# Optimization experiments

Hardware: AMD Instinct MI355X
Metric: run time of the kernel (lower is better)

The kernel has to match this reference:

```python
import jax, jax.numpy as jnp
from jax import lax
import numpy as np

B = 1024
CH = 32          # decomp.channel
LEVEL = 3        # decomp.level
CTOT = CH * (LEVEL + 1)   # 128, ODE state dim == GRU input dim
T_POINTS = 96    # decomp.eval_time_points
PRED_LEN = 96
HID = 128


def _dopri5_traj(y0, ts, Wo, bo):
    """Fixed-grid Dormand-Prince 5(4) integration of dy/dt = tanh(y Wo^T + bo).
    y0: [B, CTOT]; ts: [T]. Returns trajectory [T, B, CTOT]."""
    f = lambda y: jnp.tanh(y @ Wo.T + bo)

    def step(y, dt):
        k1 = f(y)
        k2 = f(y + dt * (0.2 * k1))
        k3 = f(y + dt * (3.0 / 40 * k1 + 9.0 / 40 * k2))
        k4 = f(y + dt * (44.0 / 45 * k1 - 56.0 / 15 * k2 + 32.0 / 9 * k3))
        k5 = f(y + dt * (19372.0 / 6561 * k1 - 25360.0 / 2187 * k2 + 64448.0 / 6561 * k3 - 212.0 / 729 * k4))
        k6 = f(y + dt * (9017.0 / 3168 * k1 - 355.0 / 33 * k2 + 46732.0 / 5247 * k3 + 49.0 / 176 * k4 - 5103.0 / 18656 * k5))
        y_next = y + dt * (35.0 / 384 * k1 + 500.0 / 1113 * k3 + 125.0 / 192 * k4 - 2187.0 / 6784 * k5 + 11.0 / 84 * k6)
        return y_next, y_next

    _, ys = lax.scan(step, y0, ts[1:] - ts[:-1])
    return jnp.concatenate([y0[None], ys], axis=0)


def _gru_layer(xs, W_ih, W_hh, b_ih, b_hh):
    """PyTorch-semantics GRU layer. xs: [T, B, D] -> hidden states [T, B, H]."""
    gi = jnp.einsum('tbd,gd->tbg', xs, W_ih) + b_ih  # precompute input gates
    H = W_hh.shape[1]

    def cell(h, gi_t):
        gh = h @ W_hh.T + b_hh
        i_r, i_z, i_n = jnp.split(gi_t, 3, axis=-1)
        h_r, h_z, h_n = jnp.split(gh, 3, axis=-1)
        r = jax.nn.sigmoid(i_r + h_r)
        z = jax.nn.sigmoid(i_z + h_z)
        n = jnp.tanh(i_n + r * h_n)
        h_new = (1.0 - z) * n + z * h
        return h_new, h_new

    h0 = jnp.zeros((xs.shape[1], H), xs.dtype)
    _, hs = lax.scan(cell, h0, gi)
    return hs


def setup_inputs() -> dict:
    key = jax.random.key(0)
    ks = jax.random.split(key, 20)
    s = 0.08  # ~1/sqrt(128), keeps GRU/ODE in a stable regime
    return {
        'x': jax.random.normal(ks[0], (B, CH, 256), jnp.float32),
        'yl': jax.random.normal(ks[1], (B, CH, 1), jnp.float32),
        'yh': jax.random.normal(ks[2], (B, CH * LEVEL, 1), jnp.float32),
        'W_ode': jax.random.normal(ks[3], (CTOT, CTOT), jnp.float32) * 0.05,
        'b_ode': jax.random.normal(ks[4], (CTOT,), jnp.float32) * 0.05,
        'W_ih0': jax.random.normal(ks[5], (3 * HID, CTOT), jnp.float32) * s,
        'W_hh0': jax.random.normal(ks[6], (3 * HID, HID), jnp.float32) * s,
        'b_ih0': jax.random.normal(ks[7], (3 * HID,), jnp.float32) * s,
        'b_hh0': jax.random.normal(ks[8], (3 * HID,), jnp.float32) * s,
        'W_ih1': jax.random.normal(ks[9], (3 * HID, HID), jnp.float32) * s,
        'W_hh1': jax.random.normal(ks[10], (3 * HID, HID), jnp.float32) * s,
        'b_ih1': jax.random.normal(ks[11], (3 * HID,), jnp.float32) * s,
        'b_hh1': jax.random.normal(ks[12], (3 * HID,), jnp.float32) * s,
        'W1': jax.random.normal(ks[13], (64, HID), jnp.float32) * s,
        'b1': jax.random.normal(ks[14], (64,), jnp.float32) * s,
        'W2': jax.random.normal(ks[15], (PRED_LEN * CH, 64), jnp.float32) * 0.125,
        'b2': jax.random.normal(ks[16], (PRED_LEN * CH,), jnp.float32) * 0.125,
    }


def reference(x, yl, yh, W_ode, b_ode,
              W_ih0, W_hh0, b_ih0, b_hh0,
              W_ih1, W_hh1, b_ih1, b_hh1,
              W1, b1, W2, b2):
    # coeffs = cat([yl] + yh, dim=1) -> [B, CTOT, 1] -> squeeze coeff length (=1)
    coeffs = jnp.concatenate([yl, yh], axis=1)[..., 0]  # [B, CTOT]
    ts = jnp.linspace(0.0, 1.0, T_POINTS)
    traj = _dopri5_traj(coeffs, ts, W_ode, b_ode)  # [T, B, CTOT]
    # rearrange 't b c l -> b t (c l)' with l == 1; GRU scans over leading T axis
    h1 = _gru_layer(traj, W_ih0, W_hh0, b_ih0, b_hh0)   # [T, B, HID]
    h2 = _gru_layer(h1, W_ih1, W_hh1, b_ih1, b_hh1)     # [T, B, HID]
    last = h2[-1]                                        # [B, HID]
    hidden = jax.nn.gelu(last @ W1.T + b1, approximate=False)
    pred = hidden @ W2.T + b2                            # [B, PRED_LEN*CH]
    return pred.reshape(-1, CH, PRED_LEN)
```

## Files before the change

### kernel.cpp

```cpp
#include <hip/hip_runtime.h>
#include <hip/hip_bf16.h>
#include <math.h>

#define TPTS 96
#define CTOT 128
#define LDP 134

typedef __bf16 bf16x8_t __attribute__((ext_vector_type(8)));
typedef float f32x4_t __attribute__((ext_vector_type(4)));
typedef unsigned short us8_t __attribute__((ext_vector_type(8)));

__device__ __forceinline__ unsigned short f2b(float f) {
    union { float f; unsigned int i; } v; v.f = f;
    unsigned int r = v.i + 0x7fffu + ((v.i >> 16) & 1u);
    return (unsigned short)(r >> 16);
}
__device__ __forceinline__ unsigned int packbf2(float a, float b) {
    unsigned int r;
    asm("v_cvt_pk_bf16_f32 %0, %1, %2" : "=v"(r) : "v"(a), "v"(b));
    return r;
}
__device__ __forceinline__ uint2 pack4(float v0, float v1, float v2, float v3) {
    uint2 w; w.x = packbf2(v0, v1); w.y = packbf2(v2, v3); return w;
}
__device__ __forceinline__ f32x4_t mfma16(bf16x8_t a, bf16x8_t b, f32x4_t c) {
    return __builtin_amdgcn_mfma_f32_16x16x32_bf16(a, b, c, 0, 0, 0);
}
__device__ __forceinline__ bf16x8_t ldfrag(const unsigned short* p) {
    us8_t v = *(const us8_t*)p;
    return __builtin_bit_cast(bf16x8_t, v);
}
__device__ __forceinline__ bf16x8_t ldfragG(const unsigned short* p) {
    union { unsigned long long q[2]; us8_t v; } u;
    u.q[0] = __hip_atomic_load((const unsigned long long*)p,
                               __ATOMIC_RELAXED, __HIP_MEMORY_SCOPE_AGENT);
    u.q[1] = __hip_atomic_load((const unsigned long long*)(p + 4),
                               __ATOMIC_RELAXED, __HIP_MEMORY_SCOPE_AGENT);
    return __builtin_bit_cast(bf16x8_t, u.v);
}
__device__ __forceinline__ void stg8(unsigned short* p, uint2 pk) {
    unsigned long long q = ((unsigned long long)pk.y << 32) | (unsigned long long)pk.x;
    __hip_atomic_store((unsigned long long*)p, q,
                       __ATOMIC_RELAXED, __HIP_MEMORY_SCOPE_AGENT);
}
__device__ __forceinline__ bf16x8_t ldfragW(const float* p) {
    float4 a = *(const float4*)p;
    float4 b = *(const float4*)(p + 4);
    bf16x8_t r;
    r[0] = __builtin_bit_cast(__bf16, f2b(a.x)); r[1] = __builtin_bit_cast(__bf16, f2b(a.y));
    r[2] = __builtin_bit_cast(__bf16, f2b(a.z)); r[3] = __builtin_bit_cast(__bf16, f2b(a.w));
    r[4] = __builtin_bit_cast(__bf16, f2b(b.x)); r[5] = __builtin_bit_cast(__bf16, f2b(b.y));
    r[6] = __builtin_bit_cast(__bf16, f2b(b.z)); r[7] = __builtin_bit_cast(__bf16, f2b(b.w));
    return r;
}
__device__ __forceinline__ float tanh2(float x) {
    float e = __expf(x + x);
    return 1.f - __fdividef(2.f, e + 1.f);
}
__device__ __forceinline__ float sigm(float x) {
    return __fdividef(1.f, 1.f + __expf(-x));
}

#define LGKM_BAR() do {                                         \
        asm volatile("s_waitcnt lgkmcnt(0)" ::: "memory");      \
        __builtin_amdgcn_s_barrier();                           \
    } while (0)

__device__ __forceinline__ void waitflag(unsigned int* f, unsigned int want) {
    if (threadIdx.x == 0) {
        int guard = 0;
        while (__hip_atomic_load(f, __ATOMIC_RELAXED, __HIP_MEMORY_SCOPE_AGENT) != want) {
            __builtin_amdgcn_s_sleep(1);
            if (++guard > (1 << 22)) break;
        }
    }
    __syncthreads();
}
__device__ __forceinline__ void setflag(unsigned int* f, unsigned int val) {
    if (threadIdx.x == 0) {
        asm volatile("s_waitcnt vmcnt(0)" ::: "memory");
        __hip_atomic_store(f, val, __ATOMIC_RELAXED, __HIP_MEMORY_SCOPE_AGENT);
    }
}

__global__ void __launch_bounds__(512, 2)
ode_forecaster(const float* __restrict__ yl,
               const float* __restrict__ yh,
               const float* __restrict__ Wode,
               const float* __restrict__ bode,
               const float* __restrict__ Wih0,
               const float* __restrict__ Whh0,
               const float* __restrict__ bih0,
               const float* __restrict__ bhh0,
               const float* __restrict__ Wih1,
               const float* __restrict__ Whh1,
               const float* __restrict__ bih1,
               const float* __restrict__ bhh1,
               const float* __restrict__ W1v,
               const float* __restrict__ b1v,
               const float* __restrict__ W2v,
               const float* __restrict__ b2v,
               float* __restrict__ outp,
               char* __restrict__ wsb)
{
    const int role = blockIdx.x >> 6;
    const int c    = blockIdx.x & 63;
    const int tid  = threadIdx.x, lane = tid & 63, wv = tid >> 6;
    const int l15  = lane & 15, quad = lane >> 4;
    const int fbase = wv * 16 + quad * 4;
    const int rbase = c * 16;

    __shared__ __align__(16) unsigned short zbuf[2][16][LDP];
    __shared__ __align__(16) unsigned short hidbuf[16][72];

    unsigned short* yTraj  = (unsigned short*)(wsb);
    unsigned short* h1Traj = (unsigned short*)(wsb + 0x2000000);
    unsigned int*   yflag  = (unsigned int*)(wsb + 0x4000000);
    unsigned int*   h1flag = (unsigned int*)(wsb + 0x4010000);
#define YMAGIC(t)  (0x5E000000u + (unsigned)(t))
#define H1MAGIC(t) (0x6E000000u + (unsigned)(t))

    if (role == 0) {
        bf16x8_t wode[4];
#pragma unroll
        for (int kt = 0; kt < 4; ++kt)
            wode[kt] = ldfragW(Wode + (wv * 16 + l15) * CTOT + kt * 32 + quad * 8);
        float bo2[4];
        {
            float4 b4 = *(const float4*)(bode + fbase);
            bo2[0] = 2.f * b4.x; bo2[1] = 2.f * b4.y; bo2[2] = 2.f * b4.z; bo2[3] = 2.f * b4.w;
        }
        float y[4];
        {
            int row = rbase + l15;
#pragma unroll
            for (int i = 0; i < 4; ++i) {
                int f = fbase + i;
                y[i] = (f < 32) ? yl[row * 32 + f] : yh[row * 96 + (f - 32)];
            }
            uint2 pk = pack4(y[0], y[1], y[2], y[3]);
            *(uint2*)&zbuf[0][l15][fbase] = pk;
            stg8(yTraj + ((size_t)row) * CTOT + fbase, pk);
        }
        __syncthreads();
        setflag(&yflag[c * 128 + 0], YMAGIC(0));

        const float dt = 1.0f / 95.0f;
        const float d10 = dt * 0.2f;
        const float d20 = dt * (3.f/40.f),  d21 = dt * (9.f/40.f);
        const float d30 = dt * (44.f/45.f), d31 = dt * (-56.f/15.f), d32 = dt * (32.f/9.f);
        const float d40 = dt * (19372.f/6561.f), d41 = dt * (-25360.f/2187.f),
                    d42 = dt * (64448.f/6561.f), d43 = dt * (-212.f/729.f);
        const float d50 = dt * (9017.f/3168.f), d51 = dt * (-355.f/33.f),
                    d52 = dt * (46732.f/5247.f), d53 = dt * (49.f/176.f),
                    d54 = dt * (-5103.f/18656.f);
        const float e0 = dt * (35.f/384.f), e2 = dt * (500.f/1113.f), e3 = dt * (125.f/192.f),
                    e4 = dt * (-2187.f/6784.f), e5 = dt * (11.f/84.f);

        int p = 0;
        float kr[6][4];
#pragma unroll 1
        for (int t = 0; t < 95; ++t) {
#pragma unroll
            for (int s = 0; s < 6; ++s) {
                bf16x8_t bf[4];
#pragma unroll
                for (int kt = 0; kt < 4; ++kt)
                    bf[kt] = ldfrag(&zbuf[p][l15][kt * 32 + quad * 8]);
                const f32x4_t zz = {0.f, 0.f, 0.f, 0.f};
                f32x4_t a0 = mfma16(wode[0], bf[0], zz);
                f32x4_t a1 = mfma16(wode[1], bf[1], zz);
                f32x4_t a2 = mfma16(wode[2], bf[2], zz);
                f32x4_t a3 = mfma16(wode[3], bf[3], zz);
                f32x4_t acc = (a0 + a1) + (a2 + a3);
#pragma unroll
                for (int i = 0; i < 4; ++i) {
                    float e = __expf(fmaf(acc[i], 2.f, bo2[i]));
                    kr[s][i] = 1.f - __fdividef(2.f, e + 1.f);
                }

                if (s < 5) {
                    float z[4];
#pragma unroll
                    for (int i = 0; i < 4; ++i) {
                        float zv;
                        if (s == 0)      zv = y[i] + d10 * kr[0][i];
                        else if (s == 1) zv = y[i] + d20 * kr[0][i] + d21 * kr[1][i];
                        else if (s == 2) zv = y[i] + d30 * kr[0][i] + d31 * kr[1][i] + d32 * kr[2][i];
                        else if (s == 3) zv = y[i] + d40 * kr[0][i] + d41 * kr[1][i]
                                             + d42 * kr[2][i] + d43 * kr[3][i];
                        else             zv = y[i] + d50 * kr[0][i] + d51 * kr[1][i]
                                             + d52 * kr[2][i] + d53 * kr[3][i] + d54 * kr[4][i];
                        z[i] = zv;
                    }
                    *(uint2*)&zbuf[p ^ 1][l15][fbase] = pack4(z[0], z[1], z[2], z[3]);
                } else {
#pragma unroll
                    for (int i = 0; i < 4; ++i)
                        y[i] += e0*kr[0][i] + e2*kr[2][i] + e3*kr[3][i] + e4*kr[4][i] + e5*kr[5][i];
                    uint2 pk = pack4(y[0], y[1], y[2], y[3]);
                    *(uint2*)&zbuf[p ^ 1][l15][fbase] = pk;
                    stg8(yTraj + ((size_t)(t + 1) * 1024 + rbase + l15) * CTOT + fbase, pk);
                }
                if (s == 1)
                    asm volatile("s_waitcnt vmcnt(0)" ::: "memory");
                LGKM_BAR();
                if (s == 1 && t > 0 && tid == 0)
                    __hip_atomic_store(&yflag[c * 128 + t], YMAGIC(t),
                                       __ATOMIC_RELAXED, __HIP_MEMORY_SCOPE_AGENT);
                p ^= 1;
            }
        }
        asm volatile("s_waitcnt vmcnt(0)" ::: "memory");
        __builtin_amdgcn_s_barrier();
        if (tid == 0)
            __hip_atomic_store(&yflag[c * 128 + 95], YMAGIC(95),
                               __ATOMIC_RELAXED, __HIP_MEMORY_SCOPE_AGENT);
        return;
    }

    const float* Wih = (role == 1) ? Wih0 : Wih1;
    const float* Whh = (role == 1) ? Whh0 : Whh1;
    const float* bih = (role == 1) ? bih0 : bih1;
    const float* bhh = (role == 1) ? bhh0 : bhh1;
    const unsigned short* src = (role == 1) ? yTraj : h1Traj;
    unsigned int* sflag = (role == 1) ? yflag : h1flag;

    bf16x8_t wih[3][4], whh[3][4];
#pragma unroll
    for (int g = 0; g < 3; ++g)
#pragma unroll
        for (int kt = 0; kt < 4; ++kt) {
            wih[g][kt] = ldfragW(Wih + (size_t)(g * 128 + wv * 16 + l15) * CTOT + kt * 32 + quad * 8);
            whh[g][kt] = ldfragW(Whh + (size_t)(g * 128 + wv * 16 + l15) * CTOT + kt * 32 + quad * 8);
        }
    float br[4], bz[4], bin_[4], bhn[4];
    {
        float4 a0 = *(const float4*)(bih + 0 * 128 + fbase);
        float4 b0 = *(const float4*)(bhh + 0 * 128 + fbase);
        float4 a1 = *(const float4*)(bih + 1 * 128 + fbase);
        float4 b1 = *(const float4*)(bhh + 1 * 128 + fbase);
        float4 a2 = *(const float4*)(bih + 2 * 128 + fbase);
        float4 b2 = *(const float4*)(bhh + 2 * 128 + fbase);
        br[0] = a0.x + b0.x; br[1] = a0.y + b0.y; br[2] = a0.z + b0.z; br[3] = a0.w + b0.w;
        bz[0] = a1.x + b1.x; bz[1] = a1.y + b1.y; bz[2] = a1.z + b1.z; bz[3] = a1.w + b1.w;
        bin_[0] = a2.x; bin_[1] = a2.y; bin_[2] = a2.z; bin_[3] = a2.w;
        bhn[0] = b2.x; bhn[1] = b2.y; bhn[2] = b2.z; bhn[3] = b2.w;
    }

    float h[4] = {0.f, 0.f, 0.f, 0.f};
    *(uint2*)&zbuf[0][l15][fbase] = pack4(0.f, 0.f, 0.f, 0.f);
    int p = 0;
    __syncthreads();

    if (role == 1) {
#pragma unroll 1
        for (int t = 0; t < TPTS; ++t) {
            asm volatile("s_waitcnt vmcnt(0)" ::: "memory");
            __builtin_amdgcn_s_barrier();
            if (tid == 0) {
                if (t > 0)
                    __hip_atomic_store(&h1flag[c * 128 + (t - 1)], H1MAGIC(t - 1),
                                       __ATOMIC_RELAXED, __HIP_MEMORY_SCOPE_AGENT);
                int guard = 0;
                while (__hip_atomic_load(&yflag[c * 128 + t],
                                         __ATOMIC_RELAXED, __HIP_MEMORY_SCOPE_AGENT) != YMAGIC(t)) {
                    __builtin_amdgcn_s_sleep(1);
                    if (++guard > (1 << 22)) break;
                }
            }
            __syncthreads();
            const unsigned short* xp = src + ((size_t)t * 1024 + rbase + l15) * CTOT;
            bf16x8_t ax[4], ah[4];
#pragma unroll
            for (int kt = 0; kt < 4; ++kt) {
                ax[kt] = ldfragG(xp + kt * 32 + quad * 8);
                ah[kt] = ldfrag(&zbuf[p][l15][kt * 32 + quad * 8]);
            }
            f32x4_t gx[3], gh[3];
#pragma unroll
            for (int g = 0; g < 3; ++g) {
                gx[g] = (f32x4_t){0.f, 0.f, 0.f, 0.f};
                gh[g] = (f32x4_t){0.f, 0.f, 0.f, 0.f};
            }
#pragma unroll
            for (int kt = 0; kt < 4; ++kt) {
                gx[0] = mfma16(wih[0][kt], ax[kt], gx[0]);
                gx[1] = mfma16(wih[1][kt], ax[kt], gx[1]);
                gx[2] = mfma16(wih[2][kt], ax[kt], gx[2]);
                gh[0] = mfma16(whh[0][kt], ah[kt], gh[0]);
                gh[1] = mfma16(whh[1][kt], ah[kt], gh[1]);
                gh[2] = mfma16(whh[2][kt], ah[kt], gh[2]);
            }
#pragma unroll
            for (int i = 0; i < 4; ++i) {
                float rr = sigm(gx[0][i] + gh[0][i] + br[i]);
                float zz = sigm(gx[1][i] + gh[1][i] + bz[i]);
                float nn = tanh2((gx[2][i] + bin_[i]) + rr * (gh[2][i] + bhn[i]));
                h[i] = nn + zz * (h[i] - nn);
            }
            uint2 pk = pack4(h[0], h[1], h[2], h[3]);
            *(uint2*)&zbuf[p ^ 1][l15][fbase] = pk;
            stg8(h1Traj + ((size_t)t * 1024 + rbase + l15) * CTOT + fbase, pk);
            LGKM_BAR();
            p ^= 1;
        }
        asm volatile("s_waitcnt vmcnt(0)" ::: "memory");
        __syncthreads();
        if (tid == 0)
            __hip_atomic_store(&h1flag[c * 128 + (TPTS - 1)], H1MAGIC(TPTS - 1),
                               __ATOMIC_RELAXED, __HIP_MEMORY_SCOPE_AGENT);
        return;
    }

#pragma unroll 1
    for (int t = 0; t < TPTS; ++t) {
        waitflag(&sflag[c * 128 + t], H1MAGIC(t));
        const unsigned short* xp = src + ((size_t)t * 1024 + rbase + l15) * CTOT;
        bf16x8_t ax[4], ah[4];
#pragma unroll
        for (int kt = 0; kt < 4; ++kt) {
            ax[kt] = ldfragG(xp + kt * 32 + quad * 8);
            ah[kt] = ldfrag(&zbuf[p][l15][kt * 32 + quad * 8]);
        }
        f32x4_t gx[3], gh[3];
#pragma unroll
        for (int g = 0; g < 3; ++g) {
            gx[g] = (f32x4_t){0.f, 0.f, 0.f, 0.f};
            gh[g] = (f32x4_t){0.f, 0.f, 0.f, 0.f};
        }
#pragma unroll
        for (int kt = 0; kt < 4; ++kt) {
            gx[0] = mfma16(wih[0][kt], ax[kt], gx[0]);
            gx[1] = mfma16(wih[1][kt], ax[kt], gx[1]);
            gx[2] = mfma16(wih[2][kt], ax[kt], gx[2]);
            gh[0] = mfma16(whh[0][kt], ah[kt], gh[0]);
            gh[1] = mfma16(whh[1][kt], ah[kt], gh[1]);
            gh[2] = mfma16(whh[2][kt], ah[kt], gh[2]);
        }
#pragma unroll
        for (int i = 0; i < 4; ++i) {
            float rr = sigm(gx[0][i] + gh[0][i] + br[i]);
            float zz = sigm(gx[1][i] + gh[1][i] + bz[i]);
            float nn = tanh2((gx[2][i] + bin_[i]) + rr * (gh[2][i] + bhn[i]));
            h[i] = nn + zz * (h[i] - nn);
        }
        *(uint2*)&zbuf[p ^ 1][l15][fbase] = pack4(h[0], h[1], h[2], h[3]);
        LGKM_BAR();
        p ^= 1;
    }

    if (wv < 4) {
        bf16x8_t wf[4], hf[4];
#pragma unroll
        for (int kt = 0; kt < 4; ++kt) {
            wf[kt] = ldfragW(W1v + (size_t)(wv * 16 + l15) * CTOT + kt * 32 + quad * 8);
            hf[kt] = ldfrag(&zbuf[p][l15][kt * 32 + quad * 8]);
        }
        f32x4_t acc = {0.f, 0.f, 0.f, 0.f};
#pragma unroll
        for (int kt = 0; kt < 4; ++kt) acc = mfma16(wf[kt], hf[kt], acc);
        float4 bb = *(const float4*)(b1v + wv * 16 + quad * 4);
        const float* bbp = (const float*)&bb;
        float gl[4];
#pragma unroll
        for (int i = 0; i < 4; ++i) {
            float x = acc[i] + bbp[i];
            gl[i] = 0.5f * x * (1.0f + erff(x * 0.70710678118654752f));
        }
        *(uint2*)&hidbuf[l15][wv * 16 + quad * 4] = pack4(gl[0], gl[1], gl[2], gl[3]);
    }
    __syncthreads();

    bf16x8_t ahid[2];
#pragma unroll
    for (int kt = 0; kt < 2; ++kt)
        ahid[kt] = ldfrag(&hidbuf[l15][kt * 32 + quad * 8]);
#pragma unroll 1
    for (int j = 0; j < 24; ++j) {
        int mt2 = wv * 24 + j;
        bf16x8_t wf0 = ldfragW(W2v + (size_t)(mt2 * 16 + l15) * 64 + quad * 8);
        bf16x8_t wf1 = ldfragW(W2v + (size_t)(mt2 * 16 + l15) * 64 + 32 + quad * 8);
        float4 bv = *(const float4*)(b2v + mt2 * 16 + quad * 4);
        const float* bvp = (const float*)&bv;
        f32x4_t acc = {0.f, 0.f, 0.f, 0.f};
        acc = mfma16(wf0, ahid[0], acc);
        acc = mfma16(wf1, ahid[1], acc);
        float4 o;
        o.x = acc[0] + bvp[0]; o.y = acc[1] + bvp[1];
        o.z = acc[2] + bvp[2]; o.w = acc[3] + bvp[3];
        *(float4*)(outp + (size_t)(rbase + l15) * 3072 + mt2 * 16 + quad * 4) = o;
    }
#undef YMAGIC
#undef H1MAGIC
}

extern "C" void kernel_launch(void* const* d_in, const int* in_sizes, int n_in,
                              void* d_out, int out_size, void* d_ws, size_t ws_size,
                              hipStream_t stream) {
    const float* yl   = (const float*)d_in[1];
    const float* yh   = (const float*)d_in[2];
    const float* Wode = (const float*)d_in[3];
    const float* bode = (const float*)d_in[4];
    const float* Wih0 = (const float*)d_in[5];
    const float* Whh0 = (const float*)d_in[6];
    const float* bih0 = (const float*)d_in[7];
    const float* bhh0 = (const float*)d_in[8];
    const float* Wih1 = (const float*)d_in[9];
    const float* Whh1 = (const float*)d_in[10];
    const float* bih1 = (const float*)d_in[11];
    const float* bhh1 = (const float*)d_in[12];
    const float* W1v  = (const float*)d_in[13];
    const float* b1v  = (const float*)d_in[14];
    const float* W2v  = (const float*)d_in[15];
    const float* b2v  = (const float*)d_in[16];

    ode_forecaster<<<dim3(192), dim3(512), 0, stream>>>(
        yl, yh, Wode, bode, Wih0, Whh0, bih0, bhh0,
        Wih1, Whh1, bih1, bhh1, W1v, b1v, W2v, b2v,
        (float*)d_out, (char*)d_ws);
}
```

Measured before the change: 764.3 us.

## Fuse ODE and first GRU layer into one 1024-thread block via LDS handoff

```diff
diff --git a/kernel.cpp b/kernel.cpp
--- a/kernel.cpp
+++ b/kernel.cpp
@@ -4,7 +4,6 @@
 
 #define TPTS 96
 #define CTOT 128
-#define LDP 134
 
 typedef __bf16 bf16x8_t __attribute__((ext_vector_type(8)));
 typedef float f32x4_t __attribute__((ext_vector_type(4)));
@@ -57,6 +56,12 @@
     float e = __expf(x + x);
     return 1.f - __fdividef(2.f, e + 1.f);
 }
+#define TWO_LOG2E 2.8853900817779268f
+__device__ __forceinline__ float tanhfast(float acc, float bl) {
+    float e = __builtin_amdgcn_exp2f(fmaf(acc, TWO_LOG2E, bl));
+    float r = __builtin_amdgcn_rcpf(e + 1.f);
+    return fmaf(-2.f, r, 1.f);
+}
 __device__ __forceinline__ float sigm(float x) {
     return __fdividef(1.f, 1.f + __expf(-x));
 }
@@ -70,20 +75,14 @@
     if (threadIdx.x == 0) {
         int guard = 0;
         while (__hip_atomic_load(f, __ATOMIC_RELAXED, __HIP_MEMORY_SCOPE_AGENT) != want) {
-            __builtin_amdgcn_s_sleep(1);
-            if (++guard > (1 << 22)) break;
+            __builtin_amdgcn_s_sleep(8);
+            if (++guard > (1 << 19)) break;
         }
     }
     __syncthreads();
 }
-__device__ __forceinline__ void setflag(unsigned int* f, unsigned int val) {
-    if (threadIdx.x == 0) {
-        asm volatile("s_waitcnt vmcnt(0)" ::: "memory");
-        __hip_atomic_store(f, val, __ATOMIC_RELAXED, __HIP_MEMORY_SCOPE_AGENT);
-    }
-}
-
-__global__ void __launch_bounds__(512, 2)
+
+__global__ void __launch_bounds__(1024, 1)
 ode_forecaster(const float* __restrict__ yl,
                const float* __restrict__ yh,
                const float* __restrict__ Wode,
@@ -103,194 +102,264 @@
                float* __restrict__ outp,
                char* __restrict__ wsb)
 {
-    const int role = blockIdx.x >> 6;
-    const int c    = blockIdx.x & 63;
-    const int tid  = threadIdx.x, lane = tid & 63, wv = tid >> 6;
-    const int l15  = lane & 15, quad = lane >> 4;
-    const int fbase = wv * 16 + quad * 4;
+    const int btype = blockIdx.x >> 6;
+    const int c     = blockIdx.x & 63;
+    const int tid   = threadIdx.x, lane = tid & 63, wv = tid >> 6;
+    const int l15   = lane & 15, quad = lane >> 4;
+    const int gw    = wv & 7;
+    const int fb    = gw * 16 + quad * 4;
     const int rbase = c * 16;
-
-    __shared__ __align__(16) unsigned short zbuf[2][16][LDP];
-    __shared__ __align__(16) unsigned short hidbuf[16][72];
-
-    unsigned short* yTraj  = (unsigned short*)(wsb);
+    const int row   = rbase + l15;
+
+    __shared__ __align__(16) char smem[25728];
+
     unsigned short* h1Traj = (unsigned short*)(wsb + 0x2000000);
-    unsigned int*   yflag  = (unsigned int*)(wsb + 0x4000000);
     unsigned int*   h1flag = (unsigned int*)(wsb + 0x4010000);
-#define YMAGIC(t)  (0x5E000000u + (unsigned)(t))
 #define H1MAGIC(t) (0x6E000000u + (unsigned)(t))
 
-    if (role == 0) {
-        bf16x8_t wode[4];
-#pragma unroll
-        for (int kt = 0; kt < 4; ++kt)
-            wode[kt] = ldfragW(Wode + (wv * 16 + l15) * CTOT + kt * 32 + quad * 8);
-        float bo2[4];
-        {
-            float4 b4 = *(const float4*)(bode + fbase);
-            bo2[0] = 2.f * b4.x; bo2[1] = 2.f * b4.y; bo2[2] = 2.f * b4.z; bo2[3] = 2.f * b4.w;
-        }
-        float y[4];
-        {
-            int row = rbase + l15;
+    if (btype == 0) {
+        unsigned short (*zb)[16][134]   = (unsigned short (*)[16][134])(smem);
+        unsigned short (*ybuf)[16][134] = (unsigned short (*)[16][134])(smem + 8576);
+        unsigned short (*hb)[16][134]   = (unsigned short (*)[16][134])(smem + 17152);
+
+        if (wv < 8) {
+            bf16x8_t wode[4];
+#pragma unroll
+            for (int kt = 0; kt < 4; ++kt)
+                wode[kt] = ldfragW(Wode + (gw * 16 + l15) * CTOT + kt * 32 + quad * 8);
+            float bl[4];
+            {
+                float4 b4 = *(const float4*)(bode + fb);
+                bl[0] = b4.x * TWO_LOG2E; bl[1] = b4.y * TWO_LOG2E;
+                bl[2] = b4.z * TWO_LOG2E; bl[3] = b4.w * TWO_LOG2E;
+            }
+            float y[4], yn[4], kr[4][4];
 #pragma unroll
             for (int i = 0; i < 4; ++i) {
-                int f = fbase + i;
+                int f = fb + i;
                 y[i] = (f < 32) ? yl[row * 32 + f] : yh[row * 96 + (f - 32)];
             }
-            uint2 pk = pack4(y[0], y[1], y[2], y[3]);
-            *(uint2*)&zbuf[0][l15][fbase] = pk;
-            stg8(yTraj + ((size_t)row) * CTOT + fbase, pk);
-        }
+            {
+                uint2 pk = pack4(y[0], y[1], y[2], y[3]);
+                *(uint2*)&zb[0][l15][fb] = pk;
+                *(uint2*)&ybuf[0][l15][fb] = pk;
+            }
+            __syncthreads();
+
+            const float dt = 1.0f / 95.0f;
+            const float d10 = dt * 0.2f;
+            const float d20 = dt * (3.f/40.f),  d21 = dt * (9.f/40.f);
+            const float d30 = dt * (44.f/45.f), d31 = dt * (-56.f/15.f), d32 = dt * (32.f/9.f);
+            const float d40 = dt * (19372.f/6561.f), d41 = dt * (-25360.f/2187.f),
+                        d42 = dt * (64448.f/6561.f), d43 = dt * (-212.f/729.f);
+            const float d50 = dt * (9017.f/3168.f), d51 = dt * (-355.f/33.f),
+                        d52 = dt * (46732.f/5247.f), d53 = dt * (49.f/176.f),
+                        d54 = dt * (-5103.f/18656.f);
+            const float e0 = dt * (35.f/384.f), e2 = dt * (500.f/1113.f), e3 = dt * (125.f/192.f),
+                        e4 = dt * (-2187.f/6784.f), e5 = dt * (11.f/84.f);
+
+            int p = 0;
+#pragma unroll 1
+            for (int T = 0; T <= 96; ++T) {
+#pragma unroll
+                for (int s = 0; s < 6; ++s) {
+                    if (T < 95) {
+                        bf16x8_t zf[4];
+#pragma unroll
+                        for (int kt = 0; kt < 4; ++kt)
+                            zf[kt] = ldfrag(&zb[p][l15][kt * 32 + quad * 8]);
+                        const f32x4_t zz4 = {0.f, 0.f, 0.f, 0.f};
+                        f32x4_t a0 = mfma16(wode[0], zf[0], zz4);
+                        f32x4_t a1 = mfma16(wode[1], zf[1], zz4);
+                        f32x4_t a2 = mfma16(wode[2], zf[2], zz4);
+                        f32x4_t a3 = mfma16(wode[3], zf[3], zz4);
+                        f32x4_t acc = (a0 + a1) + (a2 + a3);
+                        float kf[4];
+#pragma unroll
+                        for (int i = 0; i < 4; ++i) kf[i] = tanhfast(acc[i], bl[i]);
+                        if (s < 4)
+#pragma unroll
+                            for (int i = 0; i < 4; ++i) kr[s][i] = kf[i];
+#pragma unroll
+                        for (int i = 0; i < 4; ++i) {
+                            if (s == 0)      yn[i] = fmaf(e0, kf[i], y[i]);
+                            else if (s == 2) yn[i] = fmaf(e2, kf[i], yn[i]);
+                            else if (s == 3) yn[i] = fmaf(e3, kf[i], yn[i]);
+                            else if (s == 4) yn[i] = fmaf(e4, kf[i], yn[i]);
+                            else if (s == 5) y[i]  = fmaf(e5, kf[i], yn[i]);
+                        }
+                        float zv[4];
+#pragma unroll
+                        for (int i = 0; i < 4; ++i) {
+                            float zvv;
+                            if (s == 0)      zvv = fmaf(d10, kf[i], y[i]);
+                            else if (s == 1) zvv = fmaf(d21, kf[i],
+                                                    fmaf(d20, kr[0][i], y[i]));
+                            else if (s == 2) zvv = fmaf(d32, kf[i],
+                                                    fmaf(d31, kr[1][i],
+                                                    fmaf(d30, kr[0][i], y[i])));
+                            else if (s == 3) zvv = fmaf(d43, kf[i],
+                                                    fmaf(d42, kr[2][i],
+                                                    fmaf(d41, kr[1][i],
+                                                    fmaf(d40, kr[0][i], y[i]))));
+                            else if (s == 4) zvv = fmaf(d54, kf[i],
+                                                    fmaf(d53, kr[3][i],
+                                                    fmaf(d52, kr[2][i],
+                                                    fmaf(d51, kr[1][i],
+                                                    fmaf(d50, kr[0][i], y[i])))));
+                            else             zvv = y[i];
+                            zv[i] = zvv;
+                        }
+                        uint2 pk = pack4(zv[0], zv[1], zv[2], zv[3]);
+                        *(uint2*)&zb[p ^ 1][l15][fb] = pk;
+                        if (s == 5)
+                            *(uint2*)&ybuf[(T + 1) & 1][l15][fb] = pk;
+                    }
+                    LGKM_BAR();
+                    p ^= 1;
+                }
+            }
+        } else {
+            bf16x8_t wih[3][4], whh[3][4];
+#pragma unroll
+            for (int g = 0; g < 3; ++g)
+#pragma unroll
+                for (int kt = 0; kt < 4; ++kt) {
+                    wih[g][kt] = ldfragW(Wih0 + (size_t)(g * 128 + gw * 16 + l15) * CTOT + kt * 32 + quad * 8);
+                    whh[g][kt] = ldfragW(Whh0 + (size_t)(g * 128 + gw * 16 + l15) * CTOT + kt * 32 + quad * 8);
+                }
+            float br[4], bz[4], bin_[4], bhn[4];
+            {
+                float4 a0 = *(const float4*)(bih0 + 0 * 128 + fb);
+                float4 b0 = *(const float4*)(bhh0 + 0 * 128 + fb);
+                float4 a1 = *(const float4*)(bih0 + 1 * 128 + fb);
+                float4 b1 = *(const float4*)(bhh0 + 1 * 128 + fb);
+                float4 a2 = *(const float4*)(bih0 + 2 * 128 + fb);
+                float4 b2 = *(const float4*)(bhh0 + 2 * 128 + fb);
+                br[0] = a0.x + b0.x; br[1] = a0.y + b0.y; br[2] = a0.z + b0.z; br[3] = a0.w + b0.w;
+                bz[0] = a1.x + b1.x; bz[1] = a1.y + b1.y; bz[2] = a1.z + b1.z; bz[3] = a1.w + b1.w;
+                bin_[0] = a2.x; bin_[1] = a2.y; bin_[2] = a2.z; bin_[3] = a2.w;
+                bhn[0] = b2.x; bhn[1] = b2.y; bhn[2] = b2.z; bhn[3] = b2.w;
+            }
+            float h[4] = {0.f, 0.f, 0.f, 0.f};
+            *(uint2*)&hb[0][l15][fb] = pack4(0.f, 0.f, 0.f, 0.f);
+            __syncthreads();
+
+            int pg = 0;
+#pragma unroll 1
+            for (int T = 0; T <= 96; ++T) {
+                if (T >= 1) {
+                    const int t = T - 1;
+                    asm volatile("s_waitcnt vmcnt(0)" ::: "memory");
+                    bf16x8_t ax[4], ah[4];
+#pragma unroll
+                    for (int kt = 0; kt < 4; ++kt) {
+                        ax[kt] = ldfrag(&ybuf[(T - 1) & 1][l15][kt * 32 + quad * 8]);
+                        ah[kt] = ldfrag(&hb[pg][l15][kt * 32 + quad * 8]);
+                    }
+                    f32x4_t gh[3], gx[3];
+#pragma unroll
+                    for (int g = 0; g < 3; ++g) {
+                        gh[g] = (f32x4_t){0.f, 0.f, 0.f, 0.f};
+                        gx[g] = (f32x4_t){0.f, 0.f, 0.f, 0.f};
+                    }
+#pragma unroll
+                    for (int kt = 0; kt < 4; ++kt) {
+                        gh[0] = mfma16(whh[0][kt], ah[kt], gh[0]);
+                        gh[1] = mfma16(whh[1][kt], ah[kt], gh[1]);
+                        gh[2] = mfma16(whh[2][kt], ah[kt], gh[2]);
+                    }
+#pragma unroll
+                    for (int kt = 0; kt < 4; ++kt) {
+                        gx[0] = mfma16(wih[0][kt], ax[kt], gx[0]);
+                        gx[1] = mfma16(wih[1][kt], ax[kt], gx[1]);
+                        gx[2] = mfma16(wih[2][kt], ax[kt], gx[2]);
+                    }
+#pragma unroll
+                    for (int i = 0; i < 4; ++i) {
+                        float rr = sigm(gx[0][i] + gh[0][i] + br[i]);
+                        float zz = sigm(gx[1][i] + gh[1][i] + bz[i]);
+                        float nn = tanh2((gx[2][i] + bin_[i]) + rr * (gh[2][i] + bhn[i]));
+                        h[i] = nn + zz * (h[i] - nn);
+                    }
+                    uint2 pk = pack4(h[0], h[1], h[2], h[3]);
+                    *(uint2*)&hb[pg ^ 1][l15][fb] = pk;
+                    stg8(h1Traj + ((size_t)t * 1024 + row) * CTOT + fb, pk);
+                    pg ^= 1;
+                }
+                LGKM_BAR();
+                if (wv == 8 && lane == 0 && T >= 2)
+                    __hip_atomic_store(&h1flag[c * 128 + (T - 2)], H1MAGIC(T - 2),
+                                       __ATOMIC_RELAXED, __HIP_MEMORY_SCOPE_AGENT);
+#pragma unroll
+                for (int s = 1; s < 6; ++s) LGKM_BAR();
+            }
+        }
+        asm volatile("s_waitcnt vmcnt(0)" ::: "memory");
         __syncthreads();
-        setflag(&yflag[c * 128 + 0], YMAGIC(0));
-
-        const float dt = 1.0f / 95.0f;
-        const float d10 = dt * 0.2f;
-        const float d20 = dt * (3.f/40.f),  d21 = dt * (9.f/40.f);
-        const float d30 = dt * (44.f/45.f), d31 = dt * (-56.f/15.f), d32 = dt * (32.f/9.f);
-        const float d40 = dt * (19372.f/6561.f), d41 = dt * (-25360.f/2187.f),
-                    d42 = dt * (64448.f/6561.f), d43 = dt * (-212.f/729.f);
-        const float d50 = dt * (9017.f/3168.f), d51 = dt * (-355.f/33.f),
-                    d52 = dt * (46732.f/5247.f), d53 = dt * (49.f/176.f),
-                    d54 = dt * (-5103.f/18656.f);
-        const float e0 = dt * (35.f/384.f), e2 = dt * (500.f/1113.f), e3 = dt * (125.f/192.f),
-                    e4 = dt * (-2187.f/6784.f), e5 = dt * (11.f/84.f);
-
-        int p = 0;
-        float kr[6][4];
-#pragma unroll 1
-        for (int t = 0; t < 95; ++t) {
-#pragma unroll
-            for (int s = 0; s < 6; ++s) {
-                bf16x8_t bf[4];
-#pragma unroll
-                for (int kt = 0; kt < 4; ++kt)
-                    bf[kt] = ldfrag(&zbuf[p][l15][kt * 32 + quad * 8]);
-                const f32x4_t zz = {0.f, 0.f, 0.f, 0.f};
-                f32x4_t a0 = mfma16(wode[0], bf[0], zz);
-                f32x4_t a1 = mfma16(wode[1], bf[1], zz);
-                f32x4_t a2 = mfma16(wode[2], bf[2], zz);
-                f32x4_t a3 = mfma16(wode[3], bf[3], zz);
-                f32x4_t acc = (a0 + a1) + (a2 + a3);
-#pragma unroll
-                for (int i = 0; i < 4; ++i) {
-                    float e = __expf(fmaf(acc[i], 2.f, bo2[i]));
-                    kr[s][i] = 1.f - __fdividef(2.f, e + 1.f);
-                }
-
-                if (s < 5) {
-                    float z[4];
-#pragma unroll
-                    for (int i = 0; i < 4; ++i) {
-                        float zv;
-                        if (s == 0)      zv = y[i] + d10 * kr[0][i];
-                        else if (s == 1) zv = y[i] + d20 * kr[0][i] + d21 * kr[1][i];
-                        else if (s == 2) zv = y[i] + d30 * kr[0][i] + d31 * kr[1][i] + d32 * kr[2][i];
-                        else if (s == 3) zv = y[i] + d40 * kr[0][i] + d41 * kr[1][i]
-                                             + d42 * kr[2][i] + d43 * kr[3][i];
-                        else             zv = y[i] + d50 * kr[0][i] + d51 * kr[1][i]
-                                             + d52 * kr[2][i] + d53 * kr[3][i] + d54 * kr[4][i];
-                        z[i] = zv;
-                    }
-                    *(uint2*)&zbuf[p ^ 1][l15][fbase] = pack4(z[0], z[1], z[2], z[3]);
-                } else {
-#pragma unroll
-                    for (int i = 0; i < 4; ++i)
-                        y[i] += e0*kr[0][i] + e2*kr[2][i] + e3*kr[3][i] + e4*kr[4][i] + e5*kr[5][i];
-                    uint2 pk = pack4(y[0], y[1], y[2], y[3]);
-                    *(uint2*)&zbuf[p ^ 1][l15][fbase] = pk;
-                    stg8(yTraj + ((size_t)(t + 1) * 1024 + rbase + l15) * CTOT + fbase, pk);
-                }
-                if (s == 1)
-                    asm volatile("s_waitcnt vmcnt(0)" ::: "memory");
-                LGKM_BAR();
-                if (s == 1 && t > 0 && tid == 0)
-                    __hip_atomic_store(&yflag[c * 128 + t], YMAGIC(t),
-                                       __ATOMIC_RELAXED, __HIP_MEMORY_SCOPE_AGENT);
-                p ^= 1;
-            }
-        }
-        asm volatile("s_waitcnt vmcnt(0)" ::: "memory");
-        __builtin_amdgcn_s_barrier();
-        if (tid == 0)
-            __hip_atomic_store(&yflag[c * 128 + 95], YMAGIC(95),
+        if (wv == 8 && lane == 0)
+            __hip_atomic_store(&h1flag[c * 128 + 95], H1MAGIC(95),
                                __ATOMIC_RELAXED, __HIP_MEMORY_SCOPE_AGENT);
         return;
     }
 
-    const float* Wih = (role == 1) ? Wih0 : Wih1;
-    const float* Whh = (role == 1) ? Whh0 : Whh1;
-    const float* bih = (role == 1) ? bih0 : bih1;
-    const float* bhh = (role == 1) ? bhh0 : bhh1;
-    const unsigned short* src = (role == 1) ? yTraj : h1Traj;
-    unsigned int* sflag = (role == 1) ? yflag : h1flag;
+    unsigned short (*zbuf)[16][134] = (unsigned short (*)[16][134])(smem);
+    unsigned short (*hidbuf)[72]    = (unsigned short (*)[72])(smem + 17152);
 
     bf16x8_t wih[3][4], whh[3][4];
-#pragma unroll
-    for (int g = 0; g < 3; ++g)
-#pragma unroll
-        for (int kt = 0; kt < 4; ++kt) {
-            wih[g][kt] = ldfragW(Wih + (size_t)(g * 128 + wv * 16 + l15) * CTOT + kt * 32 + quad * 8);
-            whh[g][kt] = ldfragW(Whh + (size_t)(g * 128 + wv * 16 + l15) * CTOT + kt * 32 + quad * 8);
-        }
     float br[4], bz[4], bin_[4], bhn[4];
-    {
-        float4 a0 = *(const float4*)(bih + 0 * 128 + fbase);
-        float4 b0 = *(const float4*)(bhh + 0 * 128 + fbase);
-        float4 a1 = *(const float4*)(bih + 1 * 128 + fbase);
-        float4 b1 = *(const float4*)(bhh + 1 * 128 + fbase);
-        float4 a2 = *(const float4*)(bih + 2 * 128 + fbase);
-        float4 b2 = *(const float4*)(bhh + 2 * 128 + fbase);
+    if (wv < 8) {
+#pragma unroll
+        for (int g = 0; g < 3; ++g)
+#pragma unroll
+            for (int kt = 0; kt < 4; ++kt) {
+                wih[g][kt] = ldfragW(Wih1 + (size_t)(g * 128 + gw * 16 + l15) * CTOT + kt * 32 + quad * 8);
+                whh[g][kt] = ldfragW(Whh1 + (size_t)(g * 128 + gw * 16 + l15) * CTOT + kt * 32 + quad * 8);
+            }
+        float4 a0 = *(const float4*)(bih1 + 0 * 128 + fb);
+        float4 b0 = *(const float4*)(bhh1 + 0 * 128 + fb);
+        float4 a1 = *(const float4*)(bih1 + 1 * 128 + fb);
+        float4 b1 = *(const float4*)(bhh1 + 1 * 128 + fb);
+        float4 a2 = *(const float4*)(bih1 + 2 * 128 + fb);
+        float4 b2 = *(const float4*)(bhh1 + 2 * 128 + fb);
         br[0] = a0.x + b0.x; br[1] = a0.y + b0.y; br[2] = a0.z + b0.z; br[3] = a0.w + b0.w;
         bz[0] = a1.x + b1.x; bz[1] = a1.y + b1.y; bz[2] = a1.z + b1.z; bz[3] = a1.w + b1.w;
         bin_[0] = a2.x; bin_[1] = a2.y; bin_[2] = a2.z; bin_[3] = a2.w;
         bhn[0] = b2.x; bhn[1] = b2.y; bhn[2] = b2.z; bhn[3] = b2.w;
     }
-
     float h[4] = {0.f, 0.f, 0.f, 0.f};
-    *(uint2*)&zbuf[0][l15][fbase] = pack4(0.f, 0.f, 0.f, 0.f);
+    if (wv < 8) *(uint2*)&zbuf[0][l15][fb] = pack4(0.f, 0.f, 0.f, 0.f);
     int p = 0;
     __syncthreads();
 
-    if (role == 1) {
 #pragma unroll 1
-        for (int t = 0; t < TPTS; ++t) {
-            asm volatile("s_waitcnt vmcnt(0)" ::: "memory");
-            __builtin_amdgcn_s_barrier();
-            if (tid == 0) {
-                if (t > 0)
-                    __hip_atomic_store(&h1flag[c * 128 + (t - 1)], H1MAGIC(t - 1),
-                                       __ATOMIC_RELAXED, __HIP_MEMORY_SCOPE_AGENT);
-                int guard = 0;
-                while (__hip_atomic_load(&yflag[c * 128 + t],
-                                         __ATOMIC_RELAXED, __HIP_MEMORY_SCOPE_AGENT) != YMAGIC(t)) {
-                    __builtin_amdgcn_s_sleep(1);
-                    if (++guard > (1 << 22)) break;
-                }
-            }
-            __syncthreads();
-            const unsigned short* xp = src + ((size_t)t * 1024 + rbase + l15) * CTOT;
+    for (int t = 0; t < TPTS; ++t) {
+        waitflag(&h1flag[c * 128 + t], H1MAGIC(t));
+        if (wv < 8) {
+            const unsigned short* xp = h1Traj + ((size_t)t * 1024 + row) * CTOT;
             bf16x8_t ax[4], ah[4];
 #pragma unroll
+            for (int kt = 0; kt < 4; ++kt) ax[kt] = ldfragG(xp + kt * 32 + quad * 8);
+#pragma unroll
+            for (int kt = 0; kt < 4; ++kt)
+                ah[kt] = ldfrag(&zbuf[p][l15][kt * 32 + quad * 8]);
+            f32x4_t gh[3], gx[3];
+#pragma unroll
+            for (int g = 0; g < 3; ++g) {
+                gh[g] = (f32x4_t){0.f, 0.f, 0.f, 0.f};
+                gx[g] = (f32x4_t){0.f, 0.f, 0.f, 0.f};
+            }
+#pragma unroll
             for (int kt = 0; kt < 4; ++kt) {
-                ax[kt] = ldfragG(xp + kt * 32 + quad * 8);
-                ah[kt] = ldfrag(&zbuf[p][l15][kt * 32 + quad * 8]);
-            }
-            f32x4_t gx[3], gh[3];
-#pragma unroll
-            for (int g = 0; g < 3; ++g) {
-                gx[g] = (f32x4_t){0.f, 0.f, 0.f, 0.f};
-                gh[g] = (f32x4_t){0.f, 0.f, 0.f, 0.f};
+                gh[0] = mfma16(whh[0][kt], ah[kt], gh[0]);
+                gh[1] = mfma16(whh[1][kt], ah[kt], gh[1]);
+                gh[2] = mfma16(whh[2][kt], ah[kt], gh[2]);
             }
 #pragma unroll
             for (int kt = 0; kt < 4; ++kt) {
                 gx[0] = mfma16(wih[0][kt], ax[kt], gx[0]);
                 gx[1] = mfma16(wih[1][kt], ax[kt], gx[1]);
                 gx[2] = mfma16(wih[2][kt], ax[kt], gx[2]);
-                gh[0] = mfma16(whh[0][kt], ah[kt], gh[0]);
-                gh[1] = mfma16(whh[1][kt], ah[kt], gh[1]);
-                gh[2] = mfma16(whh[2][kt], ah[kt], gh[2]);
             }
 #pragma unroll
             for (int i = 0; i < 4; ++i) {
@@ -299,53 +368,8 @@
                 float nn = tanh2((gx[2][i] + bin_[i]) + rr * (gh[2][i] + bhn[i]));
                 h[i] = nn + zz * (h[i] - nn);
             }
-            uint2 pk = pack4(h[0], h[1], h[2], h[3]);
-            *(uint2*)&zbuf[p ^ 1][l15][fbase] = pk;
-            stg8(h1Traj + ((size_t)t * 1024 + rbase + l15) * CTOT + fbase, pk);
-            LGKM_BAR();
-            p ^= 1;
-        }
-        asm volatile("s_waitcnt vmcnt(0)" ::: "memory");
-        __syncthreads();
-        if (tid == 0)
-            __hip_atomic_store(&h1flag[c * 128 + (TPTS - 1)], H1MAGIC(TPTS - 1),
-                               __ATOMIC_RELAXED, __HIP_MEMORY_SCOPE_AGENT);
-        return;
-    }
-
-#pragma unroll 1
-    for (int t = 0; t < TPTS; ++t) {
-        waitflag(&sflag[c * 128 + t], H1MAGIC(t));
-        const unsigned short* xp = src + ((size_t)t * 1024 + rbase + l15) * CTOT;
-        bf16x8_t ax[4], ah[4];
-#pragma unroll
-        for (int kt = 0; kt < 4; ++kt) {
-            ax[kt] = ldfragG(xp + kt * 32 + quad * 8);
-            ah[kt] = ldfrag(&zbuf[p][l15][kt * 32 + quad * 8]);
-        }
-        f32x4_t gx[3], gh[3];
-#pragma unroll
-        for (int g = 0; g < 3; ++g) {
-            gx[g] = (f32x4_t){0.f, 0.f, 0.f, 0.f};
-            gh[g] = (f32x4_t){0.f, 0.f, 0.f, 0.f};
-        }
-#pragma unroll
-        for (int kt = 0; kt < 4; ++kt) {
-            gx[0] = mfma16(wih[0][kt], ax[kt], gx[0]);
-            gx[1] = mfma16(wih[1][kt], ax[kt], gx[1]);
-            gx[2] = mfma16(wih[2][kt], ax[kt], gx[2]);
-            gh[0] = mfma16(whh[0][kt], ah[kt], gh[0]);
-            gh[1] = mfma16(whh[1][kt], ah[kt], gh[1]);
-            gh[2] = mfma16(whh[2][kt], ah[kt], gh[2]);
-        }
-#pragma unroll
-        for (int i = 0; i < 4; ++i) {
-            float rr = sigm(gx[0][i] + gh[0][i] + br[i]);
-            float zz = sigm(gx[1][i] + gh[1][i] + bz[i]);
-            float nn = tanh2((gx[2][i] + bin_[i]) + rr * (gh[2][i] + bhn[i]));
-            h[i] = nn + zz * (h[i] - nn);
-        }
-        *(uint2*)&zbuf[p ^ 1][l15][fbase] = pack4(h[0], h[1], h[2], h[3]);
+            *(uint2*)&zbuf[p ^ 1][l15][fb] = pack4(h[0], h[1], h[2], h[3]);
+        }
         LGKM_BAR();
         p ^= 1;
     }
@@ -372,26 +396,27 @@
     }
     __syncthreads();
 
-    bf16x8_t ahid[2];
-#pragma unroll
-    for (int kt = 0; kt < 2; ++kt)
-        ahid[kt] = ldfrag(&hidbuf[l15][kt * 32 + quad * 8]);
+    if (wv < 8) {
+        bf16x8_t ahid[2];
+#pragma unroll
+        for (int kt = 0; kt < 2; ++kt)
+            ahid[kt] = ldfrag(&hidbuf[l15][kt * 32 + quad * 8]);
 #pragma unroll 1
-    for (int j = 0; j < 24; ++j) {
-        int mt2 = wv * 24 + j;
-        bf16x8_t wf0 = ldfragW(W2v + (size_t)(mt2 * 16 + l15) * 64 + quad * 8);
-        bf16x8_t wf1 = ldfragW(W2v + (size_t)(mt2 * 16 + l15) * 64 + 32 + quad * 8);
-        float4 bv = *(const float4*)(b2v + mt2 * 16 + quad * 4);
-        const float* bvp = (const float*)&bv;
-        f32x4_t acc = {0.f, 0.f, 0.f, 0.f};
-        acc = mfma16(wf0, ahid[0], acc);
-        acc = mfma16(wf1, ahid[1], acc);
-        float4 o;
-        o.x = acc[0] + bvp[0]; o.y = acc[1] + bvp[1];
-        o.z = acc[2] + bvp[2]; o.w = acc[3] + bvp[3];
-        *(float4*)(outp + (size_t)(rbase + l15) * 3072 + mt2 * 16 + quad * 4) = o;
-    }
-#undef YMAGIC
+        for (int j = 0; j < 24; ++j) {
+            int mt2 = wv * 24 + j;
+            bf16x8_t wf0 = ldfragW(W2v + (size_t)(mt2 * 16 + l15) * 64 + quad * 8);
+            bf16x8_t wf1 = ldfragW(W2v + (size_t)(mt2 * 16 + l15) * 64 + 32 + quad * 8);
+            float4 bv = *(const float4*)(b2v + mt2 * 16 + quad * 4);
+            const float* bvp = (const float*)&bv;
+            f32x4_t acc = {0.f, 0.f, 0.f, 0.f};
+            acc = mfma16(wf0, ahid[0], acc);
+            acc = mfma16(wf1, ahid[1], acc);
+            float4 o;
+            o.x = acc[0] + bvp[0]; o.y = acc[1] + bvp[1];
+            o.z = acc[2] + bvp[2]; o.w = acc[3] + bvp[3];
+            *(float4*)(outp + (size_t)row * 3072 + mt2 * 16 + quad * 4) = o;
+        }
+    }
 #undef H1MAGIC
 }
 
@@ -415,7 +440,7 @@
     const float* W2v  = (const float*)d_in[15];
     const float* b2v  = (const float*)d_in[16];
 
-    ode_forecaster<<<dim3(192), dim3(512), 0, stream>>>(
+    ode_forecaster<<<dim3(128), dim3(1024), 0, stream>>>(
         yl, yh, Wode, bode, Wih0, Whh0, bih0, bhh0,
         Wih1, Whh1, bih1, bhh1, W1v, b1v, W2v, b2v,
         (float*)d_out, (char*)d_ws);
```

After: 1.187 ms. +55.4%, slower.
